# Kernel tuning notes

Measured on AMD Instinct MI355X. Metric: run time of the kernel, lower is better.

The kernel has to match this reference:

```python
import jax, jax.numpy as jnp
import numpy as np

KERNEL_MUL = 2.0
KERNEL_NUM = 5
EPS = 1e-5


def _gaussian_kernel(a, b):
    # a: [n, d], b: [m, d]. Squared L2 distances via dot-product trick
    # (same math as the tiled (n,m,d) subtraction in the original, without
    # materializing the rank-3 intermediate).
    sq_a = jnp.sum(a * a, axis=1)  # [n]
    sq_b = jnp.sum(b * b, axis=1)  # [m]
    d2 = sq_a[:, None] + sq_b[None, :] - 2.0 * (a @ b.T)  # [n, m]
    d2 = jnp.maximum(d2, 0.0)
    n_samples = a.shape[0] + b.shape[0]
    # bandwidth from detached distances (L2_distance.data in torch)
    bw = jax.lax.stop_gradient(jnp.sum(d2)) / (n_samples ** 2 - n_samples)
    bw = bw / (KERNEL_MUL ** (KERNEL_NUM // 2))
    bws = bw * (KERNEL_MUL ** jnp.arange(KERNEL_NUM, dtype=d2.dtype)) + EPS  # [K]
    # sum of K Gaussian kernels, fused over the bandwidth axis
    k = jnp.sum(jnp.exp(-d2[None, :, :] / bws[:, None, None]), axis=0)  # [n, m]
    return k


def setup_inputs() -> dict:
    key = jax.random.key(0)
    kx, ky = jax.random.split(key)
    x = jax.random.normal(kx, (4096, 256), dtype=jnp.float32)
    y = jax.random.normal(ky, (4096, 256), dtype=jnp.float32)
    return {"x": x, "y": y}


def reference(x, y):
    xx = _gaussian_kernel(x, x).mean()
    yy = _gaussian_kernel(y, y).mean()
    xy = _gaussian_kernel(x, y).mean()
    mmd = xx + yy - 2.0 * xy
    return mmd
```

## Files before the change

kernel.cpp:

```cpp
#include <hip/hip_runtime.h>

#define N 4096
#define D 256
#define BT 128
#define NB2 32
#define TRI 528
#define TOTAL 2080
#define BK 32
#define KT (D / BK)

typedef __attribute__((ext_vector_type(8))) _Float16 f16x8;
typedef __attribute__((ext_vector_type(4))) _Float16 f16x4;
typedef __attribute__((ext_vector_type(4))) float f32x4;

__device__ __forceinline__ void gld_lds16(const void* g, void* l) {
    __builtin_amdgcn_global_load_lds(
        (const __attribute__((address_space(1))) unsigned int*)g,
        (__attribute__((address_space(3))) unsigned int*)l, 16, 0, 0);
}

__global__ void k_cvt(const float* __restrict__ x, const float* __restrict__ y,
                      _Float16* __restrict__ xc, _Float16* __restrict__ yc,
                      float* __restrict__ sq, double* __restrict__ cs) {
    const int mat = blockIdx.y;
    if (blockIdx.x == 0) cs[mat * D + threadIdx.x] = 0.0;
    const float* src = mat ? y : x;
    _Float16* dst = mat ? yc : xc;
    const int row = blockIdx.x * 4 + (threadIdx.x >> 6);
    const int lane = threadIdx.x & 63;
    const float4 v = *(const float4*)(src + (size_t)row * D + lane * 4);
    f16x4 h;
    h.x = (_Float16)v.x; h.y = (_Float16)v.y; h.z = (_Float16)v.z; h.w = (_Float16)v.w;
    *(f16x4*)(dst + (size_t)row * D + lane * 4) = h;
    float s = v.x * v.x + v.y * v.y + v.z * v.z + v.w * v.w;
    #pragma unroll
    for (int off = 32; off; off >>= 1) s += __shfl_down(s, off);
    if (lane == 0) sq[mat * N + row] = s;
}

__global__ void k_colsum(const float* __restrict__ x, const float* __restrict__ y,
                         double* __restrict__ cs) {
    const int mat = blockIdx.y;
    const float* p = (mat ? y : x);
    const int t = threadIdx.x;
    const int r0 = blockIdx.x * 32;
    float s = 0.f;
    #pragma unroll 8
    for (int r = 0; r < 32; ++r) s += p[(size_t)(r0 + r) * D + t];
    atomicAdd(&cs[mat * D + t], (double)s);
}

__global__ void k_prep(const float* __restrict__ sq, const double* __restrict__ cs,
                       float* __restrict__ coef, double* __restrict__ acc) {
    const int t = threadIdx.x;
    double sx = 0, sy = 0;
    for (int i = t; i < N; i += 256) { sx += (double)sq[i]; sy += (double)sq[N + i]; }
    const double cx = cs[t], cy = cs[D + t];
    double v[5] = {sx, sy, cx * cx, cy * cy, cx * cy};
    #pragma unroll
    for (int k = 0; k < 5; ++k)
        for (int off = 32; off; off >>= 1) v[k] += __shfl_down(v[k], off);
    __shared__ double red[4][5];
    const int w = t >> 6, lane = t & 63;
    if (lane == 0) for (int k = 0; k < 5; ++k) red[w][k] = v[k];
    __syncthreads();
    if (t == 0) {
        double Sx = 0, Sy = 0, Cxx = 0, Cyy = 0, Cxy = 0;
        for (int q = 0; q < 4; ++q) {
            Sx += red[q][0]; Sy += red[q][1];
            Cxx += red[q][2]; Cyy += red[q][3]; Cxy += red[q][4];
        }
        const double ns = 2.0 * N;
        const double denom = ns * ns - ns;
        const double sd[3] = {
            2.0 * N * Sx - 2.0 * Cxx,
            2.0 * N * Sy - 2.0 * Cyy,
            (double)N * Sx + (double)N * Sy - 2.0 * Cxy };
        const double L2E = 1.4426950408889634;
        for (int p = 0; p < 3; ++p) {
            const double bw = sd[p] / denom / 4.0;
            coef[p] = (float)(L2E / (16.0 * bw + 1e-5));
        }
        acc[0] = 0.0; acc[1] = 0.0; acc[2] = 0.0;
    }
}

__global__ __launch_bounds__(256) void k_mmd(
    const _Float16* __restrict__ xc, const _Float16* __restrict__ yc,
    const float* __restrict__ sq, const float* __restrict__ coefs,
    double* __restrict__ acc) {
    __shared__ __align__(16) _Float16 As[BT * BK];
    __shared__ __align__(16) _Float16 Bs[BT * BK];
    __shared__ double red[4];

    const int bid = (blockIdx.x & 7) * (TOTAL / 8) + (blockIdx.x >> 3);

    int p, b;
    if (bid < TRI)          { p = 0; b = bid; }
    else if (bid < 2 * TRI) { p = 1; b = bid - TRI; }
    else                    { p = 2; b = bid - 2 * TRI; }
    const _Float16* A = (p == 1) ? yc : xc;
    const _Float16* B = (p == 0) ? xc : yc;
    const float* sqA = (p == 1) ? sq + N : sq;
    const float* sqB = (p == 0) ? sq : sq + N;
    const float c4 = coefs[p];

    int bi, bj;
    if (p < 2) {
        int rem = b, r = 0;
        while (rem >= NB2 - r) { rem -= NB2 - r; ++r; }
        bi = r; bj = r + rem;
    } else { bi = b >> 5; bj = b & 31; }

    const int tid = threadIdx.x;
    const int srow = tid >> 2;
    const int sc = (tid & 3) ^ (srow & 3);
    const char* gA = (const char*)A + (size_t)(bi * BT + srow) * (D * 2) + sc * 16;
    const char* gB = (const char*)B + (size_t)(bj * BT + srow) * (D * 2) + sc * 16;
    char* lA = (char*)As + tid * 16;
    char* lB = (char*)Bs + tid * 16;

    const int lane = tid & 63, w = tid >> 6;
    const int wr = (w >> 1) * 64, wc = (w & 1) * 64;
    const int fr = lane & 15;
    const int lg = lane >> 4;
    const int ch = (lg ^ (fr & 3)) * 16;
    const char* rA = (const char*)As + (wr + fr) * 64 + ch;
    const char* rB = (const char*)Bs + (wc + fr) * 64 + ch;

    f32x4 accv[4][4];
    #pragma unroll
    for (int m = 0; m < 4; ++m)
        #pragma unroll
        for (int n = 0; n < 4; ++n) accv[m][n] = {0.f, 0.f, 0.f, 0.f};

    for (int kt = 0; kt < KT; ++kt) {
        const int kb = kt * (BK * 2);
        __syncthreads();
        gld_lds16(gA + kb, lA);
        gld_lds16(gA + kb + 64 * (D * 2), lA + 4096);
        gld_lds16(gB + kb, lB);
        gld_lds16(gB + kb + 64 * (D * 2), lB + 4096);
        __syncthreads();
        f16x8 af[4], bf[4];
        #pragma unroll
        for (int m = 0; m < 4; ++m)
            af[m] = *(const f16x8*)(rA + m * 1024);
        #pragma unroll
        for (int n = 0; n < 4; ++n)
            bf[n] = *(const f16x8*)(rB + n * 1024);
        #pragma unroll
        for (int m = 0; m < 4; ++m)
            #pragma unroll
            for (int n = 0; n < 4; ++n)
                accv[m][n] = __builtin_amdgcn_mfma_f32_16x16x32_f16(
                    af[m], bf[n], accv[m][n], 0, 0, 0);
    }

    const float c2x = 2.f * c4;
    const int row0 = bi * BT + wr + (lane >> 4) * 4;
    const int col0 = bj * BT + wc + fr;
    float asa[4][4], bsb[4];
    #pragma unroll
    for (int m = 0; m < 4; ++m) {
        const f32x4 sa = *(const f32x4*)(sqA + row0 + m * 16);
        #pragma unroll
        for (int i = 0; i < 4; ++i) asa[m][i] = sa[i] * c4;
    }
    #pragma unroll
    for (int n = 0; n < 4; ++n) bsb[n] = sqB[col0 + n * 16] * c4;
    float s = 0.f;
    #pragma unroll
    for (int m = 0; m < 4; ++m)
        #pragma unroll
        for (int n = 0; n < 4; ++n)
            #pragma unroll
            for (int i = 0; i < 4; ++i) {
                float arg = fmaf(accv[m][n][i], c2x, -(asa[m][i] + bsb[n]));
                arg = fminf(arg, 0.f);
                const float u = __builtin_amdgcn_exp2f(arg);
                const float u2 = u * u, u4 = u2 * u2;
                const float u8 = u4 * u4, u16 = u8 * u8;
                s += (u + u2) + (u4 + u8) + u16;
            }
    if (p < 2 && bi != bj) s *= 2.f;

    double sd = (double)s;
    #pragma unroll
    for (int off = 32; off; off >>= 1) sd += __shfl_down(sd, off);
    if (lane == 0) red[w] = sd;
    __syncthreads();
    if (tid == 0) atomicAdd(&acc[p], red[0] + red[1] + red[2] + red[3]);
}

__global__ void k_final(const double* __restrict__ acc, float* __restrict__ out) {
    const double inv = 1.0 / ((double)N * (double)N);
    out[0] = (float)((acc[0] + acc[1] - 2.0 * acc[2]) * inv);
}

extern "C" void kernel_launch(void* const* d_in, const int* in_sizes, int n_in,
                              void* d_out, int out_size, void* d_ws, size_t ws_size,
                              hipStream_t stream) {
    const float* x = (const float*)d_in[0];
    const float* y = (const float*)d_in[1];
    float* out = (float*)d_out;

    double* wsd = (double*)d_ws;
    double* acc = wsd;
    double* cs  = wsd + 8;
    float*  sq  = (float*)(wsd + 520);
    float*  coef = sq + 2 * N;
    char* base = (char*)d_ws;
    _Float16* xc = (_Float16*)(base + 40960);
    _Float16* yc = (_Float16*)(base + 40960 + (size_t)N * D * 2);

    k_cvt<<<dim3(N / 4, 2), 256, 0, stream>>>(x, y, xc, yc, sq, cs);
    k_colsum<<<dim3(N / 32, 2), 256, 0, stream>>>(x, y, cs);
    k_prep<<<1, 256, 0, stream>>>(sq, cs, coef, acc);
    k_mmd<<<TOTAL, 256, 0, stream>>>(xc, yc, sq, coef, acc);
    k_final<<<1, 1, 0, stream>>>(acc, out);
}
```

Measured before the change: 116.9 us.

## Double-buffer LDS tiles in MMD GEMM and fuse colsum into conversion kernel

The main kernel now double-buffers the A/B tiles in LDS, prefetching the next K-slice while MFMAs run on the current one, and drops one of the two barriers per iteration. The LDS swizzle gains an extra XOR term to reduce bank conflicts. The separate column-sum kernel is folded into the conversion kernel: each block handles 32 rows, reduces column sums through LDS and issues one atomic per column, with a memset replacing the in-kernel zeroing. The cost is twice the LDS per block, which may lower occupancy, plus an extra memset call.

New measurement: 116.2 us. About the same (-0.6%).

```diff
diff --git a/kernel.cpp b/kernel.cpp
--- a/kernel.cpp
+++ b/kernel.cpp
@@ -23,31 +23,31 @@
                       _Float16* __restrict__ xc, _Float16* __restrict__ yc,
                       float* __restrict__ sq, double* __restrict__ cs) {
     const int mat = blockIdx.y;
-    if (blockIdx.x == 0) cs[mat * D + threadIdx.x] = 0.0;
     const float* src = mat ? y : x;
     _Float16* dst = mat ? yc : xc;
-    const int row = blockIdx.x * 4 + (threadIdx.x >> 6);
-    const int lane = threadIdx.x & 63;
-    const float4 v = *(const float4*)(src + (size_t)row * D + lane * 4);
-    f16x4 h;
-    h.x = (_Float16)v.x; h.y = (_Float16)v.y; h.z = (_Float16)v.z; h.w = (_Float16)v.w;
-    *(f16x4*)(dst + (size_t)row * D + lane * 4) = h;
-    float s = v.x * v.x + v.y * v.y + v.z * v.z + v.w * v.w;
-    #pragma unroll
-    for (int off = 32; off; off >>= 1) s += __shfl_down(s, off);
-    if (lane == 0) sq[mat * N + row] = s;
-}
-
-__global__ void k_colsum(const float* __restrict__ x, const float* __restrict__ y,
-                         double* __restrict__ cs) {
-    const int mat = blockIdx.y;
-    const float* p = (mat ? y : x);
+    const int w = threadIdx.x >> 6, lane = threadIdx.x & 63;
+    const int r0 = blockIdx.x * 32 + w * 8;
+    __shared__ float lds[4][256];
+    float4 colacc = {0.f, 0.f, 0.f, 0.f};
+    #pragma unroll
+    for (int r = 0; r < 8; ++r) {
+        const int row = r0 + r;
+        const float4 v = *(const float4*)(src + (size_t)row * D + lane * 4);
+        f16x4 h;
+        h.x = (_Float16)v.x; h.y = (_Float16)v.y;
+        h.z = (_Float16)v.z; h.w = (_Float16)v.w;
+        *(f16x4*)(dst + (size_t)row * D + lane * 4) = h;
+        float s = v.x * v.x + v.y * v.y + v.z * v.z + v.w * v.w;
+        #pragma unroll
+        for (int off = 32; off; off >>= 1) s += __shfl_down(s, off);
+        if (lane == 0) sq[mat * N + row] = s;
+        colacc.x += v.x; colacc.y += v.y; colacc.z += v.z; colacc.w += v.w;
+    }
+    *(float4*)&lds[w][lane * 4] = colacc;
+    __syncthreads();
     const int t = threadIdx.x;
-    const int r0 = blockIdx.x * 32;
-    float s = 0.f;
-    #pragma unroll 8
-    for (int r = 0; r < 32; ++r) s += p[(size_t)(r0 + r) * D + t];
-    atomicAdd(&cs[mat * D + t], (double)s);
+    const float part = lds[0][t] + lds[1][t] + lds[2][t] + lds[3][t];
+    atomicAdd(&cs[mat * D + t], (double)part);
 }
 
 __global__ void k_prep(const float* __restrict__ sq, const double* __restrict__ cs,
@@ -77,9 +77,9 @@
             2.0 * N * Sy - 2.0 * Cyy,
             (double)N * Sx + (double)N * Sy - 2.0 * Cxy };
         const double L2E = 1.4426950408889634;
-        for (int p = 0; p < 3; ++p) {
-            const double bw = sd[p] / denom / 4.0;
-            coef[p] = (float)(L2E / (16.0 * bw + 1e-5));
+        for (int q = 0; q < 3; ++q) {
+            const double bw = sd[q] / denom / 4.0;
+            coef[q] = (float)(L2E / (16.0 * bw + 1e-5));
         }
         acc[0] = 0.0; acc[1] = 0.0; acc[2] = 0.0;
     }
@@ -89,8 +89,8 @@
     const _Float16* __restrict__ xc, const _Float16* __restrict__ yc,
     const float* __restrict__ sq, const float* __restrict__ coefs,
     double* __restrict__ acc) {
-    __shared__ __align__(16) _Float16 As[BT * BK];
-    __shared__ __align__(16) _Float16 Bs[BT * BK];
+    __shared__ __align__(16) _Float16 As[2 * BT * BK];
+    __shared__ __align__(16) _Float16 Bs[2 * BT * BK];
     __shared__ double red[4];
 
     const int bid = (blockIdx.x & 7) * (TOTAL / 8) + (blockIdx.x >> 3);
@@ -114,7 +114,7 @@
 
     const int tid = threadIdx.x;
     const int srow = tid >> 2;
-    const int sc = (tid & 3) ^ (srow & 3);
+    const int sc = (tid & 3) ^ (srow & 3) ^ ((srow >> 2) & 3);
     const char* gA = (const char*)A + (size_t)(bi * BT + srow) * (D * 2) + sc * 16;
     const char* gB = (const char*)B + (size_t)(bj * BT + srow) * (D * 2) + sc * 16;
     char* lA = (char*)As + tid * 16;
@@ -124,7 +124,7 @@
     const int wr = (w >> 1) * 64, wc = (w & 1) * 64;
     const int fr = lane & 15;
     const int lg = lane >> 4;
-    const int ch = (lg ^ (fr & 3)) * 16;
+    const int ch = (lg ^ (fr & 3) ^ (fr >> 2)) * 16;
     const char* rA = (const char*)As + (wr + fr) * 64 + ch;
     const char* rB = (const char*)Bs + (wc + fr) * 64 + ch;
 
@@ -134,31 +134,42 @@
         #pragma unroll
         for (int n = 0; n < 4; ++n) accv[m][n] = {0.f, 0.f, 0.f, 0.f};
 
+    gld_lds16(gA, lA);
+    gld_lds16(gA + 64 * (D * 2), lA + 4096);
+    gld_lds16(gB, lB);
+    gld_lds16(gB + 64 * (D * 2), lB + 4096);
+    __syncthreads();
+
+    #pragma unroll
     for (int kt = 0; kt < KT; ++kt) {
-        const int kb = kt * (BK * 2);
-        __syncthreads();
-        gld_lds16(gA + kb, lA);
-        gld_lds16(gA + kb + 64 * (D * 2), lA + 4096);
-        gld_lds16(gB + kb, lB);
-        gld_lds16(gB + kb + 64 * (D * 2), lB + 4096);
-        __syncthreads();
+        const int c = kt & 1;
+        if (kt + 1 < KT) {
+            const int kb = (kt + 1) * (BK * 2);
+            const int co = (c ^ 1) * 8192;
+            gld_lds16(gA + kb, lA + co);
+            gld_lds16(gA + kb + 64 * (D * 2), lA + co + 4096);
+            gld_lds16(gB + kb, lB + co);
+            gld_lds16(gB + kb + 64 * (D * 2), lB + co + 4096);
+        }
+        const int co = c * 8192;
         f16x8 af[4], bf[4];
         #pragma unroll
         for (int m = 0; m < 4; ++m)
-            af[m] = *(const f16x8*)(rA + m * 1024);
+            af[m] = *(const f16x8*)(rA + co + m * 1024);
         #pragma unroll
         for (int n = 0; n < 4; ++n)
-            bf[n] = *(const f16x8*)(rB + n * 1024);
+            bf[n] = *(const f16x8*)(rB + co + n * 1024);
         #pragma unroll
         for (int m = 0; m < 4; ++m)
             #pragma unroll
             for (int n = 0; n < 4; ++n)
                 accv[m][n] = __builtin_amdgcn_mfma_f32_16x16x32_f16(
                     af[m], bf[n], accv[m][n], 0, 0, 0);
+        if (kt + 1 < KT) __syncthreads();
     }
 
     const float c2x = 2.f * c4;
-    const int row0 = bi * BT + wr + (lane >> 4) * 4;
+    const int row0 = bi * BT + wr + lg * 4;
     const int col0 = bj * BT + wc + fr;
     float asa[4][4], bsb[4];
     #pragma unroll
@@ -214,8 +225,8 @@
     _Float16* xc = (_Float16*)(base + 40960);
     _Float16* yc = (_Float16*)(base + 40960 + (size_t)N * D * 2);
 
-    k_cvt<<<dim3(N / 4, 2), 256, 0, stream>>>(x, y, xc, yc, sq, cs);
-    k_colsum<<<dim3(N / 32, 2), 256, 0, stream>>>(x, y, cs);
+    hipMemsetAsync(cs, 0, 512 * sizeof(double), stream);
+    k_cvt<<<dim3(N / 32, 2), 256, 0, stream>>>(x, y, xc, yc, sq, cs);
     k_prep<<<1, 256, 0, stream>>>(sq, cs, coef, acc);
     k_mmd<<<TOTAL, 256, 0, stream>>>(xc, yc, sq, coef, acc);
     k_final<<<1, 1, 0, stream>>>(acc, out);
```
